# Kernel optimization log

Measured on AMD Instinct MI355X. Metric: run time of the kernel, lower is better.

The kernel has to match this reference:

```python
import jax, jax.numpy as jnp
import numpy as np


def _build_R(angles, mus):
    """Build n x n orthonormal matrix from n(n-1)/2 Givens angles, then scale rows by mus.
    Rotation order matches SaivDr's OrthonormalMatrixGenerationSystem: iTop outer, iBtm inner.
    """
    n = mus.shape[0]
    top_np, btm_np = np.triu_indices(n, k=1)  # row-major pair order (0,1),(0,2),...,(n-2,n-1)
    top = jnp.asarray(top_np, dtype=jnp.int32)
    btm = jnp.asarray(btm_np, dtype=jnp.int32)
    c = jnp.cos(angles)
    s = jnp.sin(angles)

    def step(R, cstb):
        ci, si, t, b = cstb
        rt = R[t]
        rb = R[b]
        R = R.at[t].set(ci * rt - si * rb)
        R = R.at[b].set(si * rt + ci * rb)
        return R, None

    R0 = jnp.eye(n, dtype=angles.dtype)
    R, _ = jax.lax.scan(step, R0, (c, s, top, btm))
    return mus[:, None] * R


def setup_inputs() -> dict:
    key = jax.random.key(0)
    k1, k2 = jax.random.split(key)
    n, m = 64, 1_000_000
    X = jax.random.normal(k1, (n, m), dtype=jnp.float32)
    angles = jax.random.normal(k2, (n * (n - 1) // 2,), dtype=jnp.float32)
    mus = jnp.ones((n,), dtype=jnp.float32)
    return {"X": X, "angles": angles, "mus": mus}


def reference(X, angles, mus):
    # OrthonormalTransform, mode='Analysis': out = R @ X
    R = _build_R(angles, mus)
    return R @ X
```

## Files before the change

kernel.cpp:

```cpp
#include <hip/hip_runtime.h>
#include <math.h>

#define N 64
#define NPAIRS (N * (N - 1) / 2)

__global__ __launch_bounds__(64) void build_r_kernel(
    const float* __restrict__ angles, const float* __restrict__ mus,
    float* __restrict__ RT) {
  __shared__ float2 cs[NPAIRS];
  const int lane = threadIdx.x;

  for (int k = lane; k < NPAIRS; k += 64) {
    float a = angles[k];
    float s, c;
    sincosf(a, &s, &c);
    cs[k] = make_float2(c, s);
  }
  __syncthreads();

  float col[N];
#pragma unroll
  for (int i = 0; i < N; ++i) col[i] = (i == lane) ? 1.0f : 0.0f;

  int k = 0;
#pragma unroll
  for (int t = 0; t < N - 1; ++t) {
#pragma unroll
    for (int b = t + 1; b < N; ++b) {
      float2 p = cs[k++];
      float rt = col[t];
      float rb = col[b];
      col[t] = fmaf(p.x, rt, -p.y * rb);
      col[b] = fmaf(p.y, rt, p.x * rb);
    }
  }

#pragma unroll
  for (int i = 0; i < N; ++i) {
    RT[lane * N + i] = mus[i] * col[i];
  }
}

__global__ __launch_bounds__(256) void apply_r_kernel(
    const float* __restrict__ X, const float* __restrict__ RT,
    float* __restrict__ out, int m) {
  const int j = blockIdx.x * 256 + threadIdx.x;
  if (j >= m) return;

  float acc[N];
#pragma unroll
  for (int i = 0; i < N; ++i) acc[i] = 0.0f;

  const float* xp = X + j;
#pragma unroll 4
  for (int k = 0; k < N; ++k) {
    const float x = xp[(size_t)k * m];
    const float4* r4 = (const float4*)(RT + k * N);
#pragma unroll
    for (int ii = 0; ii < N / 4; ++ii) {
      float4 r = r4[ii];
      acc[ii * 4 + 0] = fmaf(r.x, x, acc[ii * 4 + 0]);
      acc[ii * 4 + 1] = fmaf(r.y, x, acc[ii * 4 + 1]);
      acc[ii * 4 + 2] = fmaf(r.z, x, acc[ii * 4 + 2]);
      acc[ii * 4 + 3] = fmaf(r.w, x, acc[ii * 4 + 3]);
    }
  }

#pragma unroll
  for (int i = 0; i < N; ++i) {
    out[(size_t)i * m + j] = acc[i];
  }
}

extern "C" void kernel_launch(void* const* d_in, const int* in_sizes, int n_in,
                              void* d_out, int out_size, void* d_ws,
                              size_t ws_size, hipStream_t stream) {
  const float* X = (const float*)d_in[0];
  const float* angles = (const float*)d_in[1];
  const float* mus = (const float*)d_in[2];
  float* out = (float*)d_out;
  float* RT = (float*)d_ws;

  const int m = in_sizes[0] / N;

  build_r_kernel<<<1, 64, 0, stream>>>(angles, mus, RT);

  const int blocks = (m + 255) / 256;
  apply_r_kernel<<<blocks, 256, 0, stream>>>(X, RT, out, m);
}
```

Measured before the change: 476.8 us.

## Vectorize apply kernel to two columns per thread and batch Givens coefficient loads

```diff
diff --git a/kernel.cpp b/kernel.cpp
--- a/kernel.cpp
+++ b/kernel.cpp
@@ -26,12 +26,20 @@
 #pragma unroll
   for (int t = 0; t < N - 1; ++t) {
 #pragma unroll
-    for (int b = t + 1; b < N; ++b) {
-      float2 p = cs[k++];
-      float rt = col[t];
-      float rb = col[b];
-      col[t] = fmaf(p.x, rt, -p.y * rb);
-      col[b] = fmaf(p.y, rt, p.x * rb);
+    for (int b0 = t + 1; b0 < N; b0 += 8) {
+      const int nb = (N - b0) < 8 ? (N - b0) : 8;
+      float2 buf[8];
+#pragma unroll
+      for (int u = 0; u < nb; ++u) buf[u] = cs[k + u];
+#pragma unroll
+      for (int u = 0; u < nb; ++u) {
+        const int b = b0 + u;
+        const float rt = col[t];
+        const float rb = col[b];
+        col[t] = fmaf(buf[u].x, rt, -buf[u].y * rb);
+        col[b] = fmaf(buf[u].y, rt, buf[u].x * rb);
+      }
+      k += nb;
     }
   }
 
@@ -44,31 +52,37 @@
 __global__ __launch_bounds__(256) void apply_r_kernel(
     const float* __restrict__ X, const float* __restrict__ RT,
     float* __restrict__ out, int m) {
-  const int j = blockIdx.x * 256 + threadIdx.x;
-  if (j >= m) return;
+  const int m2 = m >> 1;
+  const int j2 = blockIdx.x * 256 + threadIdx.x;
+  if (j2 >= m2) return;
 
-  float acc[N];
+  float2 acc[N];
 #pragma unroll
-  for (int i = 0; i < N; ++i) acc[i] = 0.0f;
+  for (int i = 0; i < N; ++i) acc[i] = make_float2(0.0f, 0.0f);
 
-  const float* xp = X + j;
+  const float2* xp = (const float2*)X + j2;
 #pragma unroll 4
   for (int k = 0; k < N; ++k) {
-    const float x = xp[(size_t)k * m];
+    const float2 x = xp[(size_t)k * m2];
     const float4* r4 = (const float4*)(RT + k * N);
 #pragma unroll
     for (int ii = 0; ii < N / 4; ++ii) {
-      float4 r = r4[ii];
-      acc[ii * 4 + 0] = fmaf(r.x, x, acc[ii * 4 + 0]);
-      acc[ii * 4 + 1] = fmaf(r.y, x, acc[ii * 4 + 1]);
-      acc[ii * 4 + 2] = fmaf(r.z, x, acc[ii * 4 + 2]);
-      acc[ii * 4 + 3] = fmaf(r.w, x, acc[ii * 4 + 3]);
+      const float4 r = r4[ii];
+      acc[ii * 4 + 0].x = fmaf(r.x, x.x, acc[ii * 4 + 0].x);
+      acc[ii * 4 + 0].y = fmaf(r.x, x.y, acc[ii * 4 + 0].y);
+      acc[ii * 4 + 1].x = fmaf(r.y, x.x, acc[ii * 4 + 1].x);
+      acc[ii * 4 + 1].y = fmaf(r.y, x.y, acc[ii * 4 + 1].y);
+      acc[ii * 4 + 2].x = fmaf(r.z, x.x, acc[ii * 4 + 2].x);
+      acc[ii * 4 + 2].y = fmaf(r.z, x.y, acc[ii * 4 + 2].y);
+      acc[ii * 4 + 3].x = fmaf(r.w, x.x, acc[ii * 4 + 3].x);
+      acc[ii * 4 + 3].y = fmaf(r.w, x.y, acc[ii * 4 + 3].y);
     }
   }
 
+  float2* op = (float2*)out + j2;
 #pragma unroll
   for (int i = 0; i < N; ++i) {
-    out[(size_t)i * m + j] = acc[i];
+    op[(size_t)i * m2] = acc[i];
   }
 }
 
@@ -82,9 +96,10 @@
   float* RT = (float*)d_ws;
 
   const int m = in_sizes[0] / N;
+  const int m2 = m >> 1;
 
   build_r_kernel<<<1, 64, 0, stream>>>(angles, mus, RT);
 
-  const int blocks = (m + 255) / 256;
+  const int blocks = (m2 + 255) / 256;
   apply_r_kernel<<<blocks, 256, 0, stream>>>(X, RT, out, m);
 }
```

New measurement: 645.8 us. 1.35x slower.
